# Kernel optimization log

Measured on AMD Instinct MI355X. Metric: run time of the kernel, lower is better.

The kernel has to match this reference:

```python
import jax, jax.numpy as jnp
import numpy as np
import math

# batch, in-channels, attention_maps, heads, features (== input height), frames
B, C, M, H, F_, W = 2, 8, 8, 8, 256, 512
HD = F_ // H  # head dim = 32


def conv2d(x, w, pad):
    return jax.lax.conv_general_dilated(x, w, (1, 1), pad,
                                        dimension_numbers=('NCHW', 'OIHW', 'NCHW'))


def rotary(x):
    # lucidrains-style interleaved rotary over last dim; x: [..., seq, d]
    d, seq = x.shape[-1], x.shape[-2]
    inv_freq = 1.0 / (10000.0 ** (jnp.arange(0, d, 2, dtype=jnp.float32) / d))
    freqs = jnp.arange(seq, dtype=jnp.float32)[:, None] * inv_freq[None, :]  # [seq, d/2]
    freqs = jnp.repeat(freqs, 2, axis=-1)  # [seq, d], each freq repeated for the (x1,x2) pair
    cos, sin = jnp.cos(freqs), jnp.sin(freqs)
    x1, x2 = x[..., 0::2], x[..., 1::2]
    xr = jnp.stack((-x2, x1), axis=-1).reshape(x.shape)  # rotate_half
    return x * cos + xr * sin


def setup_inputs() -> dict:
    key = jax.random.key(0)
    ks = jax.random.split(key, 12)
    s = 0.02
    return {
        'x': jax.random.normal(ks[0], (B, C, F_, W), jnp.float32),
        'prev_qk': jax.random.normal(ks[1], (B, M, H, W, W), jnp.float32) * 0.1,
        'q_c1': jax.random.normal(ks[2], (M, C, 3, 3), jnp.float32) * s,
        'q_lin': jax.random.normal(ks[3], (M, F_, F_), jnp.float32) * s,
        'q_c2': jax.random.normal(ks[4], (M, M, 1, 3), jnp.float32) * s,
        'k_c1': jax.random.normal(ks[5], (M, C, 3, 3), jnp.float32) * s,
        'k_lin': jax.random.normal(ks[6], (M, F_, F_), jnp.float32) * s,
        'k_c2': jax.random.normal(ks[7], (M, M, 1, 3), jnp.float32) * s,
        'v_c1': jax.random.normal(ks[8], (M, C, 3, 3), jnp.float32) * s,
        'v_lin': jax.random.normal(ks[9], (M, F_, F_), jnp.float32) * s,
        'v_c2': jax.random.normal(ks[10], (M, M, 1, 3), jnp.float32) * s,
        'o_w': jax.random.normal(ks[11], (M, F_, F_), jnp.float32) * s,
    }


def _proj(x, wc1, wl, wc2):
    h = conv2d(x, wc1, [(1, 1), (1, 1)])        # [B,M,F,W] 3x3 conv, no bias
    h = jnp.einsum('bcfw,cgf->bcgw', h, wl)      # MultichannelLinear: per-map linear on feature dim
    h = conv2d(h, wc2, [(0, 0), (1, 1)])         # (1,3) conv along frames
    return h


def _heads(t):
    # [B,M,F,W] -> transpose(2,3) -> [B,M,W,F] -> [B,M,W,H,HD] -> [B,M,H,W,HD]
    return t.transpose(0, 1, 3, 2).reshape(B, M, W, H, HD).transpose(0, 1, 3, 2, 4)


def reference(x, prev_qk, q_c1, q_lin, q_c2, k_c1, k_lin, k_c2, v_c1, v_lin, v_c2, o_w):
    q = rotary(_heads(_proj(x, q_c1, q_lin, q_c2)))
    k = rotary(_heads(_proj(x, k_c1, k_lin, k_c2)))
    v = _heads(_proj(x, v_c1, v_lin, v_c2))
    # scaled by sqrt(h) where h == input height == features (non-standard)
    qk = jnp.einsum('bmhqd,bmhkd->bmhqk', q, k) / math.sqrt(F_) + prev_qk
    a = jnp.einsum('bmhqk,bmhkd->bmhqd', jax.nn.softmax(qk, axis=-1), v)
    a = a.transpose(0, 1, 3, 2, 4).reshape(B, M, W, F_).transpose(0, 1, 3, 2)  # [B,M,F,W]
    out = jnp.einsum('bcfw,cgf->bcgw', a, o_w)  # o_proj MultichannelLinear
    return (out, qk)
```

## Files before the change

### kernel.cpp

```cpp
#include <hip/hip_runtime.h>

#define B 2
#define C 8
#define M 8
#define H 8
#define F 256
#define W 512
#define HD 32

typedef __attribute__((ext_vector_type(8))) __bf16 bf16x8;
typedef __attribute__((ext_vector_type(4))) float f32x4;

__device__ __forceinline__ unsigned short f2bf(float f) {
    unsigned int u = __float_as_uint(f);
    return (unsigned short)((u + 0x7fffu + ((u >> 16) & 1u)) >> 16);
}

__global__ __launch_bounds__(256) void conv1_kernel(const float* __restrict__ x,
                                                    const float* __restrict__ w0,
                                                    const float* __restrict__ w1,
                                                    const float* __restrict__ w2,
                                                    float* __restrict__ out) {
    int t = threadIdx.x;
    int zb = blockIdx.z;
    int b = zb >> 3, m = zb & 7;
    int wi = blockIdx.x * 64 + (t & 63);
    int f0t = blockIdx.y * 32 + (t >> 6) * 8;
    const float* xb = x + (size_t)b * C * F * W;
    const float* wq = w0 + m * 72;
    const float* wk = w1 + m * 72;
    const float* wv = w2 + m * 72;
    int wm = (wi > 0) ? wi - 1 : 0;
    int wp = (wi < W - 1) ? wi + 1 : W - 1;
    bool e0 = (wi > 0), e1 = (wi < W - 1);
    float acc[3][8] = {};
    for (int i = 0; i < 8; ++i) {
        const float* xi = xb + (size_t)i * F * W;
        float v0[10], v1[10], v2[10];
        #pragma unroll
        for (int rr = 0; rr < 10; ++rr) {
            int ff = f0t + rr - 1;
            if (ff >= 0 && ff < F) {
                const float* xr = xi + (size_t)ff * W;
                float a = xr[wm], bb = xr[wi], c = xr[wp];
                v0[rr] = e0 ? a : 0.f;
                v1[rr] = bb;
                v2[rr] = e1 ? c : 0.f;
            } else {
                v0[rr] = 0.f; v1[rr] = 0.f; v2[rr] = 0.f;
            }
        }
        #pragma unroll
        for (int p = 0; p < 3; ++p) {
            const float* wt = ((p == 0) ? wq : (p == 1) ? wk : wv) + i * 9;
            #pragma unroll
            for (int df = 0; df < 3; ++df) {
                float s0 = wt[df * 3 + 0];
                float s1 = wt[df * 3 + 1];
                float s2 = wt[df * 3 + 2];
                #pragma unroll
                for (int ff = 0; ff < 8; ++ff)
                    acc[p][ff] += v0[ff + df] * s0 + v1[ff + df] * s1 + v2[ff + df] * s2;
            }
        }
    }
    #pragma unroll
    for (int p = 0; p < 3; ++p) {
        size_t zo = (size_t)(p * 16 + zb) * F;
        #pragma unroll
        for (int ff = 0; ff < 8; ++ff)
            out[(zo + f0t + ff) * W + wi] = acc[p][ff];
    }
}

__global__ __launch_bounds__(256) void lin_kernel(const float* __restrict__ in,
                                                  const float* __restrict__ w0,
                                                  const float* __restrict__ w1,
                                                  const float* __restrict__ w2,
                                                  float* __restrict__ out) {
    __shared__ float As[32][68];
    __shared__ float Bs[32][68];
    int t = threadIdx.x;
    int z = blockIdx.z;
    int proj = z >> 4, m = z & 7;
    const float* wsel = (proj == 0) ? w0 : (proj == 1) ? w1 : w2;
    const float* wm = wsel + (size_t)m * F * F;
    const float* ib = in + (size_t)z * F * W;
    float* ob = out + (size_t)z * F * W;
    int g0 = blockIdx.y * 64, wb0 = blockIdx.x * 64;
    int ty = t >> 4, tx = t & 15;
    int gg = t >> 2, fq = (t & 3) * 8;
    int lkk = t >> 3, wq = (t & 7) * 8;
    float4 a0 = *(const float4*)&wm[(size_t)(g0 + gg) * F + fq];
    float4 a1 = *(const float4*)&wm[(size_t)(g0 + gg) * F + fq + 4];
    float4 b0 = *(const float4*)&ib[(size_t)lkk * W + wb0 + wq];
    float4 b1 = *(const float4*)&ib[(size_t)lkk * W + wb0 + wq + 4];
    float acc[4][4] = {};
    for (int f0 = 0; f0 < F; f0 += 32) {
        As[fq + 0][gg] = a0.x; As[fq + 1][gg] = a0.y; As[fq + 2][gg] = a0.z; As[fq + 3][gg] = a0.w;
        As[fq + 4][gg] = a1.x; As[fq + 5][gg] = a1.y; As[fq + 6][gg] = a1.z; As[fq + 7][gg] = a1.w;
        *(float4*)&Bs[lkk][wq] = b0;
        *(float4*)&Bs[lkk][wq + 4] = b1;
        __syncthreads();
        if (f0 + 32 < F) {
            a0 = *(const float4*)&wm[(size_t)(g0 + gg) * F + f0 + 32 + fq];
            a1 = *(const float4*)&wm[(size_t)(g0 + gg) * F + f0 + 32 + fq + 4];
            b0 = *(const float4*)&ib[(size_t)(f0 + 32 + lkk) * W + wb0 + wq];
            b1 = *(const float4*)&ib[(size_t)(f0 + 32 + lkk) * W + wb0 + wq + 4];
        }
        #pragma unroll
        for (int kk = 0; kk < 32; ++kk) {
            float4 a4 = *(const float4*)&As[kk][ty * 4];
            float4 b4 = *(const float4*)&Bs[kk][tx * 4];
            acc[0][0] += a4.x * b4.x; acc[0][1] += a4.x * b4.y; acc[0][2] += a4.x * b4.z; acc[0][3] += a4.x * b4.w;
            acc[1][0] += a4.y * b4.x; acc[1][1] += a4.y * b4.y; acc[1][2] += a4.y * b4.z; acc[1][3] += a4.y * b4.w;
            acc[2][0] += a4.z * b4.x; acc[2][1] += a4.z * b4.y; acc[2][2] += a4.z * b4.z; acc[2][3] += a4.z * b4.w;
            acc[3][0] += a4.w * b4.x; acc[3][1] += a4.w * b4.y; acc[3][2] += a4.w * b4.z; acc[3][3] += a4.w * b4.w;
        }
        __syncthreads();
    }
    #pragma unroll
    for (int i = 0; i < 4; ++i) {
        float4 o = make_float4(acc[i][0], acc[i][1], acc[i][2], acc[i][3]);
        *(float4*)&ob[(size_t)(g0 + ty * 4 + i) * W + wb0 + tx * 4] = o;
    }
}

__global__ __launch_bounds__(256) void conv2_heads_kernel(const float* __restrict__ in,
                                                          const float* __restrict__ w0c,
                                                          const float* __restrict__ w1c,
                                                          const float* __restrict__ w2c,
                                                          unsigned short* __restrict__ outp) {
    __shared__ float wl[192];
    __shared__ float Ot[64][65];
    int t = threadIdx.x;
    int z = blockIdx.z;
    int proj = z >> 4, bz = z & 15;
    int b = bz >> 3, o = bz & 7;
    const float* wt = (proj == 0) ? w0c : (proj == 1) ? w1c : w2c;
    int do_rot = (proj < 2);
    if (t < 192) wl[t] = wt[t];
    __syncthreads();
    int f0 = blockIdx.y * 64, w0 = blockIdx.x * 64;
    const float* ib = in + ((size_t)proj * 16 + (size_t)b * M) * F * W;
    int ww = t & 63, fq = (t >> 6) * 16;
    int w = w0 + ww;
    for (int ff = 0; ff < 16; ++ff) {
        int f = f0 + fq + ff;
        float acc = 0.f;
        #pragma unroll
        for (int i = 0; i < 8; ++i) {
            const float* r = ib + ((size_t)i * F + f) * W + w;
            float v0 = (w - 1 >= 0) ? r[-1] : 0.f;
            float v1 = r[0];
            float v2 = (w + 1 < W) ? r[1] : 0.f;
            const float* wr = &wl[(o * 8 + i) * 3];
            acc += v0 * wr[0] + v1 * wr[1] + v2 * wr[2];
        }
        Ot[fq + ff][ww] = acc;
    }
    __syncthreads();
    size_t zbase = (size_t)z * H * W * HD;
    if (do_rot) {
        for (int k = 0; k < 16; ++k) {
            int idx = k * 256 + t;
            int ddh = idx & 63;
            int wi = idx >> 6;
            int f = f0 + ddh;
            int h = f >> 5, d = f & 31;
            float e  = Ot[ddh & ~1][wi];
            float od = Ot[ddh | 1][wi];
            int jp = d >> 1;
            float invf = exp2f(-(float)jp * 0.83048202372184058f);
            float th = (float)(w0 + wi) * invf;
            float cs = __cosf(th), sn = __sinf(th);
            float val = (d & 1) ? (od * cs + e * sn) : (e * cs - od * sn);
            outp[zbase + ((size_t)h * W + (w0 + wi)) * HD + d] = f2bf(val);
        }
    } else {
        for (int k = 0; k < 16; ++k) {
            int idx = k * 256 + t;
            int wi = idx & 63;
            int ddh = idx >> 6;
            int f = f0 + ddh;
            int h = f >> 5, d = f & 31;
            outp[zbase + ((size_t)(h * HD + d)) * W + (w0 + wi)] = f2bf(Ot[ddh][wi]);
        }
    }
}

__global__ __launch_bounds__(256) void attn_kernel(const unsigned short* __restrict__ qb,
                                                   const unsigned short* __restrict__ kb,
                                                   const unsigned short* __restrict__ vtb,
                                                   const float* __restrict__ prev,
                                                   float* __restrict__ qk,
                                                   float* __restrict__ abuf) {
    __shared__ __align__(16) unsigned short VsT[32 * 520];
    __shared__ __align__(16) unsigned short PT[4][16 * 72];
    int t = threadIdx.x;
    int l = t & 63, wv = t >> 6;
    int lr = l & 15, lg = l >> 4;
    int w0 = blockIdx.x * 64;
    int bmh = blockIdx.y;
    const unsigned short* Q  = qb  + (size_t)bmh * W * HD;
    const unsigned short* K  = kb  + (size_t)bmh * W * HD;
    const unsigned short* VT = vtb + (size_t)bmh * HD * W;
    const float* P0 = prev + (size_t)bmh * W * W;
    float* QK = qk + (size_t)bmh * W * W;
    int bm = bmh >> 3, h = bmh & 7;
    float* A = abuf + ((size_t)bm * F + h * HD) * W;

    #pragma unroll
    for (int it = 0; it < 8; ++it) {
        int e16 = it * 256 + t;
        int hd = e16 >> 6, w8 = (e16 & 63) * 8;
        *(uint4*)&VsT[hd * 520 + w8] = *(const uint4*)&VT[(size_t)hd * W + w8];
    }
    int qrow = w0 + wv * 16;
    bf16x8 qf = *(const bf16x8*)&Q[(size_t)(qrow + lr) * HD + lg * 8];

    float m_i[4], l_i[4];
    f32x4 accA[2];
    #pragma unroll
    for (int r = 0; r < 4; ++r) { m_i[r] = -3.0e38f; l_i[r] = 0.f; }
    accA[0] = (f32x4)0.f;
    accA[1] = (f32x4)0.f;

    __syncthreads();

    bf16x8 kfA[4], kfB[4];
    f32x4 pvA[4], pvB[4];

    auto issue = [&](bf16x8 (&kf)[4], f32x4 (&pv)[4], int c) {
        int j0 = c * 64;
        #pragma unroll
        for (int ct = 0; ct < 4; ++ct)
            kf[ct] = *(const bf16x8*)&K[(size_t)(j0 + ct * 16 + lr) * HD + lg * 8];
        #pragma unroll
        for (int ct = 0; ct < 4; ++ct) {
            const float* pr = &P0[(size_t)(qrow + lg * 4) * W + j0 + ct * 16 + lr];
            #pragma unroll
            for (int r = 0; r < 4; ++r) pv[ct][r] = pr[(size_t)r * W];
        }
    };

    auto step = [&](bf16x8 (&kf)[4], f32x4 (&pv)[4], int c) {
        int j0 = c * 64;
        f32x4 sc[4];
        #pragma unroll
        for (int ct = 0; ct < 4; ++ct)
            sc[ct] = __builtin_amdgcn_mfma_f32_16x16x32_bf16(qf, kf[ct], pv[ct] * 16.f, 0, 0, 0);
        float sv[4][4];
        #pragma unroll
        for (int ct = 0; ct < 4; ++ct) {
            #pragma unroll
            for (int r = 0; r < 4; ++r) {
                sv[ct][r] = sc[ct][r] * 0.0625f;
                QK[(size_t)(qrow + lg * 4 + r) * W + j0 + ct * 16 + lr] = sv[ct][r];
            }
        }
        float p[4][4];
        #pragma unroll
        for (int r = 0; r < 4; ++r) {
            float cm = fmaxf(fmaxf(sv[0][r], sv[1][r]), fmaxf(sv[2][r], sv[3][r]));
            #pragma unroll
            for (int off = 1; off < 16; off <<= 1) cm = fmaxf(cm, __shfl_xor(cm, off));
            float mn = fmaxf(m_i[r], cm);
            float alpha = __expf(m_i[r] - mn);
            m_i[r] = mn;
            float rs = 0.f;
            #pragma unroll
            for (int ct = 0; ct < 4; ++ct) { p[ct][r] = __expf(sv[ct][r] - mn); rs += p[ct][r]; }
            #pragma unroll
            for (int off = 1; off < 16; off <<= 1) rs += __shfl_xor(rs, off);
            l_i[r] = l_i[r] * alpha + rs;
            accA[0][r] *= alpha;
            accA[1][r] *= alpha;
        }
        unsigned short* PTw = &PT[wv][0];
        #pragma unroll
        for (int ct = 0; ct < 4; ++ct)
            #pragma unroll
            for (int r = 0; r < 4; ++r)
                PTw[(lg * 4 + r) * 72 + ct * 16 + lr] = f2bf(p[ct][r]);
        asm volatile("s_waitcnt lgkmcnt(0)" ::: "memory");
        __builtin_amdgcn_sched_barrier(0);
        bf16x8 pf[2];
        pf[0] = *(const bf16x8*)&PTw[lr * 72 + lg * 8];
        pf[1] = *(const bf16x8*)&PTw[lr * 72 + 32 + lg * 8];
        #pragma unroll
        for (int ks = 0; ks < 2; ++ks)
            #pragma unroll
            for (int ct2 = 0; ct2 < 2; ++ct2) {
                bf16x8 vf = *(const bf16x8*)&VsT[(ct2 * 16 + lr) * 520 + j0 + ks * 32 + lg * 8];
                accA[ct2] = __builtin_amdgcn_mfma_f32_16x16x32_bf16(pf[ks], vf, accA[ct2], 0, 0, 0);
            }
    };

    issue(kfA, pvA, 0);
    #pragma unroll
    for (int cc = 0; cc < 4; ++cc) {
        issue(kfB, pvB, 2 * cc + 1);
        step(kfA, pvA, 2 * cc);
        if (cc < 3) issue(kfA, pvA, 2 * cc + 2);
        step(kfB, pvB, 2 * cc + 1);
    }

    float inv[4];
    #pragma unroll
    for (int r = 0; r < 4; ++r) inv[r] = 1.f / l_i[r];
    float* Otf = (float*)&PT[wv][0];
    asm volatile("s_waitcnt lgkmcnt(0)" ::: "memory");
    #pragma unroll
    for (int ct2 = 0; ct2 < 2; ++ct2)
        #pragma unroll
        for (int r = 0; r < 4; ++r)
            Otf[(lg * 4 + r) * 33 + ct2 * 16 + lr] = accA[ct2][r] * inv[r];
    asm volatile("s_waitcnt lgkmcnt(0)" ::: "memory");
    __builtin_amdgcn_sched_barrier(0);
    #pragma unroll
    for (int k = 0; k < 8; ++k) {
        int flat = k * 64 + l;
        int woff = flat & 15, d = flat >> 4;
        A[(size_t)d * W + w0 + wv * 16 + woff] = Otf[woff * 33 + d];
    }
}

extern "C" void kernel_launch(void* const* d_in, const int* in_sizes, int n_in,
                              void* d_out, int out_size, void* d_ws, size_t ws_size,
                              hipStream_t stream) {
    const float* x    = (const float*)d_in[0];
    const float* prev = (const float*)d_in[1];
    const float* qc1  = (const float*)d_in[2];
    const float* qlin = (const float*)d_in[3];
    const float* qc2  = (const float*)d_in[4];
    const float* kc1  = (const float*)d_in[5];
    const float* klin = (const float*)d_in[6];
    const float* kc2  = (const float*)d_in[7];
    const float* vc1  = (const float*)d_in[8];
    const float* vlin = (const float*)d_in[9];
    const float* vc2  = (const float*)d_in[10];
    const float* ow   = (const float*)d_in[11];
    float* out0  = (float*)d_out;
    float* qkout = out0 + (size_t)B * M * F * W;
    float* ws = (float*)d_ws;
    size_t n = (size_t)B * M * F * W;
    float* r1 = ws;
    float* r2 = ws + 3 * n;
    unsigned short* qkv16 = (unsigned short*)r1;

    dim3 blk(256);
    dim3 gconv1(8, 8, 16), glin3(8, 4, 48), gconv2(8, 4, 48);
    dim3 gattn(8, 128), glin1(8, 4, 16);

    conv1_kernel<<<gconv1, blk, 0, stream>>>(x, qc1, kc1, vc1, r1);
    lin_kernel<<<glin3, blk, 0, stream>>>(r1, qlin, klin, vlin, r2);
    conv2_heads_kernel<<<gconv2, blk, 0, stream>>>(r2, qc2, kc2, vc2, qkv16);
    attn_kernel<<<gattn, blk, 0, stream>>>(qkv16, qkv16 + n, qkv16 + 2 * n, prev, qkout, r2);
    lin_kernel<<<glin1, blk, 0, stream>>>(r2, ow, ow, ow, out0);
}
```

Measured before the change: 410.5 us.

## Run multichannel linear layers on bf16 MFMA with hi/lo split precision

The scalar fp32 FMA tiled GEMM in lin_kernel is replaced with bf16 MFMA 16x16x32 instructions. A three-term hi/lo split (hi*hi + hi*lo + lo*hi) keeps the result close to fp32 accuracy. Producer kernels (conv1, attn) now write activations as packed hi/lo bf16 pairs, and a new pre-kernel splits the four weight tensors every call. This trades an extra launch, weight traffic and 3x MFMA work for far higher matrix throughput.

```diff
diff --git a/kernel.cpp b/kernel.cpp
--- a/kernel.cpp
+++ b/kernel.cpp
@@ -7,6 +7,7 @@
 #define F 256
 #define W 512
 #define HD 32
+#define MFF (M * F * F)
 
 typedef __attribute__((ext_vector_type(8))) __bf16 bf16x8;
 typedef __attribute__((ext_vector_type(4))) float f32x4;
@@ -14,13 +15,42 @@
 __device__ __forceinline__ unsigned short f2bf(float f) {
     unsigned int u = __float_as_uint(f);
     return (unsigned short)((u + 0x7fffu + ((u >> 16) & 1u)) >> 16);
+}
+
+__device__ __forceinline__ unsigned int packsplit(float v) {
+    unsigned short h = f2bf(v);
+    float hf = __uint_as_float((unsigned int)h << 16);
+    unsigned short lo = f2bf(v - hf);
+    return (unsigned int)h | ((unsigned int)lo << 16);
+}
+
+__global__ __launch_bounds__(256) void wsplit_kernel(const float* __restrict__ w0,
+                                                     const float* __restrict__ w1,
+                                                     const float* __restrict__ w2,
+                                                     const float* __restrict__ w3,
+                                                     unsigned short* __restrict__ hi) {
+    int idx = blockIdx.x * 256 + threadIdx.x;
+    int set = idx >> 17;
+    int off = (idx & 131071) * 4;
+    const float* src = (set == 0) ? w0 : (set == 1) ? w1 : (set == 2) ? w2 : w3;
+    float4 v = *(const float4*)&src[off];
+    unsigned short* hp = hi + (size_t)set * MFF + off;
+    unsigned short* lp = hp + 4 * MFF;
+    ushort4 hv, lv;
+    float x;
+    x = v.x; hv.x = f2bf(x); lv.x = f2bf(x - __uint_as_float((unsigned)hv.x << 16));
+    x = v.y; hv.y = f2bf(x); lv.y = f2bf(x - __uint_as_float((unsigned)hv.y << 16));
+    x = v.z; hv.z = f2bf(x); lv.z = f2bf(x - __uint_as_float((unsigned)hv.z << 16));
+    x = v.w; hv.w = f2bf(x); lv.w = f2bf(x - __uint_as_float((unsigned)hv.w << 16));
+    *(ushort4*)hp = hv;
+    *(ushort4*)lp = lv;
 }
 
 __global__ __launch_bounds__(256) void conv1_kernel(const float* __restrict__ x,
                                                     const float* __restrict__ w0,
                                                     const float* __restrict__ w1,
                                                     const float* __restrict__ w2,
-                                                    float* __restrict__ out) {
+                                                    unsigned int* __restrict__ out) {
     int t = threadIdx.x;
     int zb = blockIdx.z;
     int b = zb >> 3, m = zb & 7;
@@ -69,61 +99,85 @@
         size_t zo = (size_t)(p * 16 + zb) * F;
         #pragma unroll
         for (int ff = 0; ff < 8; ++ff)
-            out[(zo + f0t + ff) * W + wi] = acc[p][ff];
-    }
-}
-
-__global__ __launch_bounds__(256) void lin_kernel(const float* __restrict__ in,
-                                                  const float* __restrict__ w0,
-                                                  const float* __restrict__ w1,
-                                                  const float* __restrict__ w2,
+            out[(zo + f0t + ff) * W + wi] = packsplit(acc[p][ff]);
+    }
+}
+
+__global__ __launch_bounds__(256) void lin_kernel(const unsigned int* __restrict__ in32,
+                                                  const unsigned short* __restrict__ whA,
+                                                  const unsigned short* __restrict__ whB,
+                                                  const unsigned short* __restrict__ whC,
                                                   float* __restrict__ out) {
-    __shared__ float As[32][68];
-    __shared__ float Bs[32][68];
+    __shared__ unsigned int BsH[64][20];
+    __shared__ unsigned int BsL[64][20];
     int t = threadIdx.x;
     int z = blockIdx.z;
     int proj = z >> 4, m = z & 7;
-    const float* wsel = (proj == 0) ? w0 : (proj == 1) ? w1 : w2;
-    const float* wm = wsel + (size_t)m * F * F;
-    const float* ib = in + (size_t)z * F * W;
+    const unsigned short* wh = ((proj == 0) ? whA : (proj == 1) ? whB : whC) + (size_t)m * F * F;
+    const unsigned short* wl = wh + 4 * MFF;
+    const unsigned int* ib = in32 + (size_t)z * F * W;
     float* ob = out + (size_t)z * F * W;
     int g0 = blockIdx.y * 64, wb0 = blockIdx.x * 64;
-    int ty = t >> 4, tx = t & 15;
-    int gg = t >> 2, fq = (t & 3) * 8;
-    int lkk = t >> 3, wq = (t & 7) * 8;
-    float4 a0 = *(const float4*)&wm[(size_t)(g0 + gg) * F + fq];
-    float4 a1 = *(const float4*)&wm[(size_t)(g0 + gg) * F + fq + 4];
-    float4 b0 = *(const float4*)&ib[(size_t)lkk * W + wb0 + wq];
-    float4 b1 = *(const float4*)&ib[(size_t)lkk * W + wb0 + wq + 4];
-    float acc[4][4] = {};
-    for (int f0 = 0; f0 < F; f0 += 32) {
-        As[fq + 0][gg] = a0.x; As[fq + 1][gg] = a0.y; As[fq + 2][gg] = a0.z; As[fq + 3][gg] = a0.w;
-        As[fq + 4][gg] = a1.x; As[fq + 5][gg] = a1.y; As[fq + 6][gg] = a1.z; As[fq + 7][gg] = a1.w;
-        *(float4*)&Bs[lkk][wq] = b0;
-        *(float4*)&Bs[lkk][wq + 4] = b1;
+    int wv = t >> 6, l = t & 63, lr = l & 15, lg = l >> 4;
+    int wgr = wv >> 1, wgc = wv & 1;
+    int sp = t & 15;
+    int sg = t >> 4;
+
+    uint4 ra, rb;
+    ra = *(const uint4*)&ib[(size_t)(2 * sp) * W + wb0 + sg * 4];
+    rb = *(const uint4*)&ib[(size_t)(2 * sp + 1) * W + wb0 + sg * 4];
+
+    f32x4 acc[2][2];
+    acc[0][0] = (f32x4)0.f; acc[0][1] = (f32x4)0.f;
+    acc[1][0] = (f32x4)0.f; acc[1][1] = (f32x4)0.f;
+
+    for (int s = 0; s < 8; ++s) {
+        int f0 = s * 32;
+        if (s) __syncthreads();
+        unsigned int aw[4] = {ra.x, ra.y, ra.z, ra.w};
+        unsigned int bw[4] = {rb.x, rb.y, rb.z, rb.w};
+        #pragma unroll
+        for (int j = 0; j < 4; ++j) {
+            BsH[sg * 4 + j][sp] = (aw[j] & 0xFFFFu) | (bw[j] << 16);
+            BsL[sg * 4 + j][sp] = (aw[j] >> 16) | (bw[j] & 0xFFFF0000u);
+        }
         __syncthreads();
-        if (f0 + 32 < F) {
-            a0 = *(const float4*)&wm[(size_t)(g0 + gg) * F + f0 + 32 + fq];
-            a1 = *(const float4*)&wm[(size_t)(g0 + gg) * F + f0 + 32 + fq + 4];
-            b0 = *(const float4*)&ib[(size_t)(f0 + 32 + lkk) * W + wb0 + wq];
-            b1 = *(const float4*)&ib[(size_t)(f0 + 32 + lkk) * W + wb0 + wq + 4];
-        }
-        #pragma unroll
-        for (int kk = 0; kk < 32; ++kk) {
-            float4 a4 = *(const float4*)&As[kk][ty * 4];
-            float4 b4 = *(const float4*)&Bs[kk][tx * 4];
-            acc[0][0] += a4.x * b4.x; acc[0][1] += a4.x * b4.y; acc[0][2] += a4.x * b4.z; acc[0][3] += a4.x * b4.w;
-            acc[1][0] += a4.y * b4.x; acc[1][1] += a4.y * b4.y; acc[1][2] += a4.y * b4.z; acc[1][3] += a4.y * b4.w;
-            acc[2][0] += a4.z * b4.x; acc[2][1] += a4.z * b4.y; acc[2][2] += a4.z * b4.z; acc[2][3] += a4.z * b4.w;
-            acc[3][0] += a4.w * b4.x; acc[3][1] += a4.w * b4.y; acc[3][2] += a4.w * b4.z; acc[3][3] += a4.w * b4.w;
-        }
-        __syncthreads();
-    }
-    #pragma unroll
-    for (int i = 0; i < 4; ++i) {
-        float4 o = make_float4(acc[i][0], acc[i][1], acc[i][2], acc[i][3]);
-        *(float4*)&ob[(size_t)(g0 + ty * 4 + i) * W + wb0 + tx * 4] = o;
-    }
+        if (s < 7) {
+            ra = *(const uint4*)&ib[(size_t)(f0 + 32 + 2 * sp) * W + wb0 + sg * 4];
+            rb = *(const uint4*)&ib[(size_t)(f0 + 32 + 2 * sp + 1) * W + wb0 + sg * 4];
+        }
+        bf16x8 ah[2], al[2], bh[2], bl[2];
+        #pragma unroll
+        for (int ti = 0; ti < 2; ++ti) {
+            size_t ar = (size_t)(g0 + wgr * 32 + ti * 16 + lr) * F + f0 + lg * 8;
+            ah[ti] = *(const bf16x8*)&wh[ar];
+            al[ti] = *(const bf16x8*)&wl[ar];
+        }
+        #pragma unroll
+        for (int tj = 0; tj < 2; ++tj) {
+            int wc = wgc * 32 + tj * 16 + lr;
+            bh[tj] = *(const bf16x8*)((const unsigned short*)&BsH[wc][0] + lg * 8);
+            bl[tj] = *(const bf16x8*)((const unsigned short*)&BsL[wc][0] + lg * 8);
+        }
+        #pragma unroll
+        for (int ti = 0; ti < 2; ++ti)
+            #pragma unroll
+            for (int tj = 0; tj < 2; ++tj) {
+                acc[ti][tj] = __builtin_amdgcn_mfma_f32_16x16x32_bf16(ah[ti], bh[tj], acc[ti][tj], 0, 0, 0);
+                acc[ti][tj] = __builtin_amdgcn_mfma_f32_16x16x32_bf16(ah[ti], bl[tj], acc[ti][tj], 0, 0, 0);
+                acc[ti][tj] = __builtin_amdgcn_mfma_f32_16x16x32_bf16(al[ti], bh[tj], acc[ti][tj], 0, 0, 0);
+            }
+    }
+    #pragma unroll
+    for (int ti = 0; ti < 2; ++ti)
+        #pragma unroll
+        for (int tj = 0; tj < 2; ++tj)
+            #pragma unroll
+            for (int r = 0; r < 4; ++r) {
+                int g = g0 + wgr * 32 + ti * 16 + lg * 4 + r;
+                int w = wb0 + wgc * 32 + tj * 16 + lr;
+                ob[(size_t)g * W + w] = acc[ti][tj][r];
+            }
 }
 
 __global__ __launch_bounds__(256) void conv2_heads_kernel(const float* __restrict__ in,
@@ -194,7 +248,7 @@
                                                    const unsigned short* __restrict__ vtb,
                                                    const float* __restrict__ prev,
                                                    float* __restrict__ qk,
-                                                   float* __restrict__ abuf) {
+                                                   unsigned int* __restrict__ abuf) {
     __shared__ __align__(16) unsigned short VsT[32 * 520];
     __shared__ __align__(16) unsigned short PT[4][16 * 72];
     int t = threadIdx.x;
@@ -208,7 +262,7 @@
     const float* P0 = prev + (size_t)bmh * W * W;
     float* QK = qk + (size_t)bmh * W * W;
     int bm = bmh >> 3, h = bmh & 7;
-    float* A = abuf + ((size_t)bm * F + h * HD) * W;
+    unsigned int* A = abuf + ((size_t)bm * F + h * HD) * W;
 
     #pragma unroll
     for (int it = 0; it < 8; ++it) {
@@ -322,7 +376,7 @@
     for (int k = 0; k < 8; ++k) {
         int flat = k * 64 + l;
         int woff = flat & 15, d = flat >> 4;
-        A[(size_t)d * W + w0 + wv * 16 + woff] = Otf[woff * 33 + d];
+        A[(size_t)d * W + w0 + wv * 16 + woff] = packsplit(Otf[woff * 33 + d]);
     }
 }
 
@@ -347,15 +401,19 @@
     size_t n = (size_t)B * M * F * W;
     float* r1 = ws;
     float* r2 = ws + 3 * n;
+    unsigned int* r1u = (unsigned int*)r1;
+    unsigned int* r2u = (unsigned int*)r2;
     unsigned short* qkv16 = (unsigned short*)r1;
+    unsigned short* whi = (unsigned short*)(ws + 6 * n);
 
     dim3 blk(256);
-    dim3 gconv1(8, 8, 16), glin3(8, 4, 48), gconv2(8, 4, 48);
+    dim3 gsplit(2048), gconv1(8, 8, 16), glin3(8, 4, 48), gconv2(8, 4, 48);
     dim3 gattn(8, 128), glin1(8, 4, 16);
 
-    conv1_kernel<<<gconv1, blk, 0, stream>>>(x, qc1, kc1, vc1, r1);
-    lin_kernel<<<glin3, blk, 0, stream>>>(r1, qlin, klin, vlin, r2);
+    wsplit_kernel<<<gsplit, blk, 0, stream>>>(qlin, klin, vlin, ow, whi);
+    conv1_kernel<<<gconv1, blk, 0, stream>>>(x, qc1, kc1, vc1, r1u);
+    lin_kernel<<<glin3, blk, 0, stream>>>(r1u, whi, whi + MFF, whi + 2 * MFF, r2);
     conv2_heads_kernel<<<gconv2, blk, 0, stream>>>(r2, qc2, kc2, vc2, qkv16);
-    attn_kernel<<<gattn, blk, 0, stream>>>(qkv16, qkv16 + n, qkv16 + 2 * n, prev, qkout, r2);
-    lin_kernel<<<glin1, blk, 0, stream>>>(r2, ow, ow, ow, out0);
-}
+    attn_kernel<<<gattn, blk, 0, stream>>>(qkv16, qkv16 + n, qkv16 + 2 * n, prev, qkout, r2u);
+    lin_kernel<<<glin1, blk, 0, stream>>>(r2u, whi + 3 * MFF, whi + 3 * MFF, whi + 3 * MFF, out0);
+}
```

Result: faster. 398.8 us (-2.9%).
